# Kernel optimization log

Hardware: AMD Instinct MI355X
Metric: run time of the kernel (lower is better)

## Reference

```python
import jax, jax.numpy as jnp
import numpy as np

EPS = 1e-5
N, DEG, D, L = 50000, 16, 128, 2  # nodes, max_neighbor, embed_size, gnn_layer


def _log_map_zero(y):
    # Poincare ball log map at origin: atanh(||y||) * y / ||y||, with clamps
    n = jnp.linalg.norm(y, axis=-1, keepdims=True)
    nc = jnp.clip(n, EPS, 1.0 - EPS)
    return y * (jnp.arctanh(nc) / nc)


def _exp_map_zero(v):
    # Poincare ball exp map at origin: tanh(||v||) * v / ||v||
    n = jnp.linalg.norm(v, axis=-1, keepdims=True)
    nc = jnp.maximum(n, EPS)
    return v * (jnp.tanh(nc) / nc)


def setup_inputs() -> dict:
    key = jax.random.key(0)
    k1, k2, k3, k4, k5 = jax.random.split(key, 5)
    node_repr = jax.random.normal(k1, (N, D), jnp.float32) * 0.1
    adj = jax.random.randint(k2, (N, DEG), 0, N)
    weight = jax.random.normal(k3, (N, DEG), jnp.float32)
    mask = jnp.ones((N, 1), jnp.float32)
    # per-relation, per-layer message weights (2 relations: pos / neg edges)
    scale = 1.0 / np.sqrt(D)
    W_pos = jax.random.normal(k4, (L, D, D), jnp.float32) * scale
    W_neg = jax.random.normal(k5, (L, D, D), jnp.float32) * scale
    return {"node_repr": node_repr, "adj": adj, "weight": weight,
            "mask": mask, "W_pos": W_pos, "W_neg": W_neg}


def reference(node_repr, adj, weight, mask, W_pos, W_neg):
    # split_graph_by_negative_edge
    pos_m = (weight > 0).astype(weight.dtype)
    neg_m = (weight < 0).astype(weight.dtype)
    adjs = (adj * pos_m.astype(adj.dtype), adj * neg_m.astype(adj.dtype))
    ws = (weight * pos_m, (-weight) * neg_m)
    Ws = (W_pos, W_neg)

    x = node_repr
    for step in range(L):
        x = (_log_map_zero(x) if step > 0 else x) * mask
        combined = jnp.zeros_like(x)
        for a, w, W in zip(adjs, ws, Ws):
            msg = (x @ W[step]) * mask                    # [N, D]
            nb = msg[a.reshape(-1)].reshape(N, DEG, D)    # neighbor gather
            combined = combined + jnp.sum(w[..., None] * nb, axis=1)
        combined = combined * mask                        # dropout identity (eval)
        x = _exp_map_zero(combined) * mask
        x = jax.nn.relu(x) * mask                         # poincare activation
    return x
```

## Files before the change

### kernel.cpp

```cpp
#include <hip/hip_runtime.h>
#include <math.h>

#define DD 128
#define DEG 16
#define TM 16
#define LDST 136
#define EPSV 1e-5f

typedef _Float16 half4_t __attribute__((ext_vector_type(4)));
typedef _Float16 half8_t __attribute__((ext_vector_type(8)));
typedef float    f32x4   __attribute__((ext_vector_type(4)));

__global__ void prep(const float* __restrict__ x, const float* __restrict__ mask,
                     _Float16* __restrict__ x16, int n4, int xb,
                     const float* __restrict__ Wp, const float* __restrict__ Wn,
                     _Float16* __restrict__ WT)
{
    if ((int)blockIdx.x < xb) {
        int i = blockIdx.x * blockDim.x + threadIdx.x;
        if (i >= n4) return;
        float m = mask[i >> 5];
        float m2 = m * m;
        float4 v = ((const float4*)x)[i];
        half4_t h;
        h[0] = (_Float16)(v.x * m2); h[1] = (_Float16)(v.y * m2);
        h[2] = (_Float16)(v.z * m2); h[3] = (_Float16)(v.w * m2);
        ((half4_t*)x16)[i] = h;
    } else {
        int bid   = blockIdx.x - xb;
        int mat   = bid >> 3;
        int chunk = bid & 7;
        int l = mat >> 1, rel = mat & 1;
        const float* __restrict__ src = (rel ? Wn : Wp) + (size_t)l * DD * DD;
        _Float16* __restrict__ dst = WT + (size_t)mat * DD * DD;
        for (int o = chunk * 2048 + threadIdx.x; o < chunk * 2048 + 2048; o += 256) {
            int nn = o >> 7, kk = o & 127;
            dst[o] = (_Float16)src[kk * DD + nn];
        }
    }
}

__global__ __launch_bounds__(256, 4) void fused_layer(
    const _Float16* __restrict__ src16,
    const int*   __restrict__ adj, const float* __restrict__ wgt,
    const float* __restrict__ mask,
    const _Float16* __restrict__ WTp, const _Float16* __restrict__ WTn,
    float* __restrict__ dst_f32, _Float16* __restrict__ dst_f16,
    int n, int apply_logmap)
{
    __shared__ __align__(16) _Float16 aggP[TM][LDST];
    __shared__ __align__(16) _Float16 aggN[TM][LDST];
    __shared__ float partA[4][TM];
    __shared__ float partB[4][TM];

    const int row0 = blockIdx.x * TM;
    const int tid  = threadIdx.x;
    const int qw   = tid >> 4;
    const int l16  = tid & 15;

    float aP[8] = {0.f,0.f,0.f,0.f,0.f,0.f,0.f,0.f};
    float aN[8] = {0.f,0.f,0.f,0.f,0.f,0.f,0.f,0.f};
    const int node = row0 + qw;
    if (node < n) {
        const int*   __restrict__ arow = adj + (size_t)node * DEG;
        const float* __restrict__ wrow = wgt + (size_t)node * DEG;
        int   idxs[16];
        float ws[16];
        #pragma unroll
        for (int b = 0; b < 4; ++b) {
            int4   ia = ((const int4*)arow)[b];
            float4 wa = ((const float4*)wrow)[b];
            idxs[b*4+0] = ia.x; idxs[b*4+1] = ia.y; idxs[b*4+2] = ia.z; idxs[b*4+3] = ia.w;
            ws[b*4+0] = wa.x; ws[b*4+1] = wa.y; ws[b*4+2] = wa.z; ws[b*4+3] = wa.w;
        }
        half8_t v[16];
        #pragma unroll
        for (int j = 0; j < 16; ++j)
            v[j] = *(const half8_t*)(src16 + (size_t)idxs[j] * DD + l16 * 8);
        #pragma unroll
        for (int j = 0; j < 16; ++j) {
            float wp = fmaxf(ws[j], 0.f);
            float wn = fmaxf(-ws[j], 0.f);
            #pragma unroll
            for (int c = 0; c < 8; ++c) {
                float f = (float)v[j][c];
                aP[c] += wp * f;
                aN[c] += wn * f;
            }
        }
    }
    half8_t hP, hN;
    #pragma unroll
    for (int c = 0; c < 8; ++c) { hP[c] = (_Float16)aP[c]; hN[c] = (_Float16)aN[c]; }
    *(half8_t*)&aggP[qw][l16 * 8] = hP;
    *(half8_t*)&aggN[qw][l16 * 8] = hN;
    __syncthreads();

    const int wv2  = tid >> 6;
    const int l64  = tid & 63;
    const int l15  = l64 & 15;
    const int quad = l64 >> 4;

    half8_t aPf[4], aNf[4];
    #pragma unroll
    for (int kb = 0; kb < 4; ++kb) {
        aPf[kb] = *(const half8_t*)&aggP[l15][kb * 32 + quad * 8];
        aNf[kb] = *(const half8_t*)&aggN[l15][kb * 32 + quad * 8];
    }

    f32x4 acc[2];
    acc[0] = (f32x4){0.f, 0.f, 0.f, 0.f};
    acc[1] = (f32x4){0.f, 0.f, 0.f, 0.f};
    #pragma unroll
    for (int t = 0; t < 2; ++t) {
        const int nb = wv2 * 2 + t;
        const _Float16* bp = WTp + (size_t)(nb * 16 + l15) * DD + quad * 8;
        const _Float16* bn = WTn + (size_t)(nb * 16 + l15) * DD + quad * 8;
        #pragma unroll
        for (int kb = 0; kb < 4; ++kb) {
            acc[t] = __builtin_amdgcn_mfma_f32_16x16x32_f16(
                aPf[kb], *(const half8_t*)(bp + kb * 32), acc[t], 0, 0, 0);
            acc[t] = __builtin_amdgcn_mfma_f32_16x16x32_f16(
                aNf[kb], *(const half8_t*)(bn + kb * 32), acc[t], 0, 0, 0);
        }
    }

    float cv0[4], cv1[4], mr[4];
    #pragma unroll
    for (int r = 0; r < 4; ++r) {
        const int rl  = quad * 4 + r;
        const int row = row0 + rl;
        float m = (row < n) ? mask[row] : 0.f;
        mr[r] = m;
        float c0 = acc[0][r] * m, c1 = acc[1][r] * m;
        cv0[r] = c0; cv1[r] = c1;
        float p = c0 * c0 + c1 * c1;
        p += __shfl_xor(p, 1); p += __shfl_xor(p, 2);
        p += __shfl_xor(p, 4); p += __shfl_xor(p, 8);
        if (l15 == 0) partA[wv2][rl] = p;
    }
    __syncthreads();

    float x0[4], x1[4];
    #pragma unroll
    for (int r = 0; r < 4; ++r) {
        const int rl = quad * 4 + r;
        float c2 = partA[0][rl] + partA[1][rl] + partA[2][rl] + partA[3][rl];
        float nc = fmaxf(sqrtf(c2), EPSV);
        float sc = tanhf(nc) / nc;
        float m  = mr[r];
        float t0 = fmaxf(cv0[r] * sc * m, 0.f) * m;
        float t1 = fmaxf(cv1[r] * sc * m, 0.f) * m;
        x0[r] = t0; x1[r] = t1;
        if (apply_logmap) {
            float p = t0 * t0 + t1 * t1;
            p += __shfl_xor(p, 1); p += __shfl_xor(p, 2);
            p += __shfl_xor(p, 4); p += __shfl_xor(p, 8);
            if (l15 == 0) partB[wv2][rl] = p;
        }
    }

    if (apply_logmap) {
        __syncthreads();
        #pragma unroll
        for (int r = 0; r < 4; ++r) {
            const int rl  = quad * 4 + r;
            const int row = row0 + rl;
            if (row >= n) continue;
            float s2  = partB[0][rl] + partB[1][rl] + partB[2][rl] + partB[3][rl];
            float nc2 = fminf(fmaxf(sqrtf(s2), EPSV), 1.f - EPSV);
            float f = (atanhf(nc2) / nc2) * mr[r] * mr[r];
            _Float16* drow = dst_f16 + (size_t)row * DD + wv2 * 32 + l15;
            drow[0]  = (_Float16)(x0[r] * f);
            drow[16] = (_Float16)(x1[r] * f);
        }
    } else {
        #pragma unroll
        for (int r = 0; r < 4; ++r) {
            const int rl  = quad * 4 + r;
            const int row = row0 + rl;
            if (row >= n) continue;
            float* drow = dst_f32 + (size_t)row * DD + wv2 * 32 + l15;
            drow[0]  = x0[r];
            drow[16] = x1[r];
        }
    }
}

extern "C" void kernel_launch(void* const* d_in, const int* in_sizes, int n_in,
                              void* d_out, int out_size, void* d_ws, size_t ws_size,
                              hipStream_t stream)
{
    const float* node_repr = (const float*)d_in[0];
    const int*   adj       = (const int*)  d_in[1];
    const float* weight    = (const float*)d_in[2];
    const float* mask      = (const float*)d_in[3];
    const float* W_pos     = (const float*)d_in[4];
    const float* W_neg     = (const float*)d_in[5];

    const int n = in_sizes[0] / DD;

    _Float16* x16 = (_Float16*)d_ws;
    _Float16* y16 = x16 + (size_t)n * DD;
    _Float16* WT  = y16 + (size_t)n * DD;

    const int n4 = n * DD / 4;
    const int xb = (n4 + 255) / 256;
    prep<<<xb + 32, 256, 0, stream>>>(node_repr, mask, x16, n4, xb,
                                      W_pos, W_neg, WT);

    dim3 grid((n + TM - 1) / TM);
    fused_layer<<<grid, 256, 0, stream>>>(x16, adj, weight, mask,
                                          WT + 0 * DD * DD, WT + 1 * DD * DD,
                                          nullptr, y16, n, 1);
    fused_layer<<<grid, 256, 0, stream>>>(y16, adj, weight, mask,
                                          WT + 2 * DD * DD, WT + 3 * DD * DD,
                                          (float*)d_out, nullptr, n, 0);
}
```

Baseline: 188.1 us.

## Halve rows per block and spread each node's gather over 32 lanes

```diff
diff --git a/kernel.cpp b/kernel.cpp
--- a/kernel.cpp
+++ b/kernel.cpp
@@ -3,7 +3,8 @@
 
 #define DD 128
 #define DEG 16
-#define TM 16
+#define TMR 8
+#define TMP 16
 #define LDST 136
 #define EPSV 1e-5f
 
@@ -40,7 +41,7 @@
     }
 }
 
-__global__ __launch_bounds__(256, 4) void fused_layer(
+__global__ __launch_bounds__(256, 6) void fused_layer(
     const _Float16* __restrict__ src16,
     const int*   __restrict__ adj, const float* __restrict__ wgt,
     const float* __restrict__ mask,
@@ -48,52 +49,59 @@
     float* __restrict__ dst_f32, _Float16* __restrict__ dst_f16,
     int n, int apply_logmap)
 {
-    __shared__ __align__(16) _Float16 aggP[TM][LDST];
-    __shared__ __align__(16) _Float16 aggN[TM][LDST];
-    __shared__ float partA[4][TM];
-    __shared__ float partB[4][TM];
-
-    const int row0 = blockIdx.x * TM;
-    const int tid  = threadIdx.x;
-    const int qw   = tid >> 4;
-    const int l16  = tid & 15;
-
-    float aP[8] = {0.f,0.f,0.f,0.f,0.f,0.f,0.f,0.f};
-    float aN[8] = {0.f,0.f,0.f,0.f,0.f,0.f,0.f,0.f};
-    const int node = row0 + qw;
+    __shared__ __align__(16) _Float16 aggP[TMP][LDST];
+    __shared__ __align__(16) _Float16 aggN[TMP][LDST];
+    __shared__ float partA[4][TMP];
+    __shared__ float partB[4][TMP];
+
+    const int row0   = blockIdx.x * TMR;
+    const int tid    = threadIdx.x;
+    const int hw     = tid >> 5;
+    const int lane32 = tid & 31;
+
+    float aP[4] = {0.f, 0.f, 0.f, 0.f};
+    float aN[4] = {0.f, 0.f, 0.f, 0.f};
+    const int node = row0 + hw;
     if (node < n) {
         const int*   __restrict__ arow = adj + (size_t)node * DEG;
         const float* __restrict__ wrow = wgt + (size_t)node * DEG;
-        int   idxs[16];
-        float ws[16];
-        #pragma unroll
-        for (int b = 0; b < 4; ++b) {
-            int4   ia = ((const int4*)arow)[b];
-            float4 wa = ((const float4*)wrow)[b];
-            idxs[b*4+0] = ia.x; idxs[b*4+1] = ia.y; idxs[b*4+2] = ia.z; idxs[b*4+3] = ia.w;
-            ws[b*4+0] = wa.x; ws[b*4+1] = wa.y; ws[b*4+2] = wa.z; ws[b*4+3] = wa.w;
-        }
-        half8_t v[16];
+        int4   ia0 = ((const int4*)arow)[0];
+        int4   ia1 = ((const int4*)arow)[1];
+        int4   ia2 = ((const int4*)arow)[2];
+        int4   ia3 = ((const int4*)arow)[3];
+        float4 wa0 = ((const float4*)wrow)[0];
+        float4 wa1 = ((const float4*)wrow)[1];
+        float4 wa2 = ((const float4*)wrow)[2];
+        float4 wa3 = ((const float4*)wrow)[3];
+        const int idxs[16] = {ia0.x, ia0.y, ia0.z, ia0.w, ia1.x, ia1.y, ia1.z, ia1.w,
+                              ia2.x, ia2.y, ia2.z, ia2.w, ia3.x, ia3.y, ia3.z, ia3.w};
+        const float ws[16] = {wa0.x, wa0.y, wa0.z, wa0.w, wa1.x, wa1.y, wa1.z, wa1.w,
+                              wa2.x, wa2.y, wa2.z, wa2.w, wa3.x, wa3.y, wa3.z, wa3.w};
+        half4_t v[16];
         #pragma unroll
         for (int j = 0; j < 16; ++j)
-            v[j] = *(const half8_t*)(src16 + (size_t)idxs[j] * DD + l16 * 8);
+            v[j] = *(const half4_t*)(src16 + (size_t)idxs[j] * DD + lane32 * 4);
         #pragma unroll
         for (int j = 0; j < 16; ++j) {
             float wp = fmaxf(ws[j], 0.f);
             float wn = fmaxf(-ws[j], 0.f);
             #pragma unroll
-            for (int c = 0; c < 8; ++c) {
+            for (int c = 0; c < 4; ++c) {
                 float f = (float)v[j][c];
                 aP[c] += wp * f;
                 aN[c] += wn * f;
             }
         }
     }
-    half8_t hP, hN;
-    #pragma unroll
-    for (int c = 0; c < 8; ++c) { hP[c] = (_Float16)aP[c]; hN[c] = (_Float16)aN[c]; }
-    *(half8_t*)&aggP[qw][l16 * 8] = hP;
-    *(half8_t*)&aggN[qw][l16 * 8] = hN;
+    half4_t hP, hN, hz;
+    #pragma unroll
+    for (int c = 0; c < 4; ++c) {
+        hP[c] = (_Float16)aP[c]; hN[c] = (_Float16)aN[c]; hz[c] = (_Float16)0.f;
+    }
+    *(half4_t*)&aggP[hw][lane32 * 4] = hP;
+    *(half4_t*)&aggN[hw][lane32 * 4] = hN;
+    *(half4_t*)&aggP[TMR + hw][lane32 * 4] = hz;
+    *(half4_t*)&aggN[TMR + hw][lane32 * 4] = hz;
     __syncthreads();
 
     const int wv2  = tid >> 6;
@@ -130,7 +138,7 @@
     for (int r = 0; r < 4; ++r) {
         const int rl  = quad * 4 + r;
         const int row = row0 + rl;
-        float m = (row < n) ? mask[row] : 0.f;
+        float m = (rl < TMR && row < n) ? mask[row] : 0.f;
         mr[r] = m;
         float c0 = acc[0][r] * m, c1 = acc[1][r] * m;
         cv0[r] = c0; cv1[r] = c1;
@@ -166,7 +174,7 @@
         for (int r = 0; r < 4; ++r) {
             const int rl  = quad * 4 + r;
             const int row = row0 + rl;
-            if (row >= n) continue;
+            if (rl >= TMR || row >= n) continue;
             float s2  = partB[0][rl] + partB[1][rl] + partB[2][rl] + partB[3][rl];
             float nc2 = fminf(fmaxf(sqrtf(s2), EPSV), 1.f - EPSV);
             float f = (atanhf(nc2) / nc2) * mr[r] * mr[r];
@@ -179,7 +187,7 @@
         for (int r = 0; r < 4; ++r) {
             const int rl  = quad * 4 + r;
             const int row = row0 + rl;
-            if (row >= n) continue;
+            if (rl >= TMR || row >= n) continue;
             float* drow = dst_f32 + (size_t)row * DD + wv2 * 32 + l15;
             drow[0]  = x0[r];
             drow[16] = x1[r];
@@ -209,7 +217,7 @@
     prep<<<xb + 32, 256, 0, stream>>>(node_repr, mask, x16, n4, xb,
                                       W_pos, W_neg, WT);
 
-    dim3 grid((n + TM - 1) / TM);
+    dim3 grid((n + TMR - 1) / TMR);
     fused_layer<<<grid, 256, 0, stream>>>(x16, adj, weight, mask,
                                           WT + 0 * DD * DD, WT + 1 * DD * DD,
                                           nullptr, y16, n, 1);
```

After: 236.3 us. 1.26x slower.

## Split neighbor gather across waves by edge subsets with LDS partial-sum reduction

Applied to the files above, without the earlier changes.

```diff
diff --git a/kernel.cpp b/kernel.cpp
--- a/kernel.cpp
+++ b/kernel.cpp
@@ -48,64 +48,73 @@
     float* __restrict__ dst_f32, _Float16* __restrict__ dst_f16,
     int n, int apply_logmap)
 {
-    __shared__ __align__(16) _Float16 aggP[TM][LDST];
-    __shared__ __align__(16) _Float16 aggN[TM][LDST];
+    __shared__ __align__(16) _Float16 aggP[4][TM][LDST];
+    __shared__ __align__(16) _Float16 aggN[4][TM][LDST];
     __shared__ float partA[4][TM];
     __shared__ float partB[4][TM];
 
-    const int row0 = blockIdx.x * TM;
-    const int tid  = threadIdx.x;
-    const int qw   = tid >> 4;
-    const int l16  = tid & 15;
-
-    float aP[8] = {0.f,0.f,0.f,0.f,0.f,0.f,0.f,0.f};
-    float aN[8] = {0.f,0.f,0.f,0.f,0.f,0.f,0.f,0.f};
-    const int node = row0 + qw;
-    if (node < n) {
-        const int*   __restrict__ arow = adj + (size_t)node * DEG;
-        const float* __restrict__ wrow = wgt + (size_t)node * DEG;
-        int   idxs[16];
-        float ws[16];
-        #pragma unroll
-        for (int b = 0; b < 4; ++b) {
-            int4   ia = ((const int4*)arow)[b];
-            float4 wa = ((const float4*)wrow)[b];
-            idxs[b*4+0] = ia.x; idxs[b*4+1] = ia.y; idxs[b*4+2] = ia.z; idxs[b*4+3] = ia.w;
-            ws[b*4+0] = wa.x; ws[b*4+1] = wa.y; ws[b*4+2] = wa.z; ws[b*4+3] = wa.w;
-        }
-        half8_t v[16];
-        #pragma unroll
-        for (int j = 0; j < 16; ++j)
-            v[j] = *(const half8_t*)(src16 + (size_t)idxs[j] * DD + l16 * 8);
-        #pragma unroll
-        for (int j = 0; j < 16; ++j) {
-            float wp = fmaxf(ws[j], 0.f);
-            float wn = fmaxf(-ws[j], 0.f);
+    const int row0   = blockIdx.x * TM;
+    const int tid    = threadIdx.x;
+    const int wv     = tid >> 6;
+    const int l64    = tid & 63;
+    const int hw     = l64 >> 5;
+    const int lane32 = l64 & 31;
+
+    const int hrow0 = row0 + hw * 8;
+    const int mnode = hrow0 + (lane32 >> 2);
+    const int moff  = (mnode < n ? mnode : 0) * DEG + 4 * wv + (lane32 & 3);
+    int   mi = adj[moff];
+    float mw = wgt[moff];
+
+    half4_t v[32];
+    #pragma unroll
+    for (int i = 0; i < 8; ++i) {
+        #pragma unroll
+        for (int j = 0; j < 4; ++j) {
+            int idx = __shfl(mi, 4 * i + j, 32);
+            v[4 * i + j] = *(const half4_t*)(src16 + (size_t)idx * DD + lane32 * 4);
+        }
+    }
+    #pragma unroll
+    for (int i = 0; i < 8; ++i) {
+        float aP[4] = {0.f, 0.f, 0.f, 0.f};
+        float aN[4] = {0.f, 0.f, 0.f, 0.f};
+        #pragma unroll
+        for (int j = 0; j < 4; ++j) {
+            float w  = __shfl(mw, 4 * i + j, 32);
+            float wp = fmaxf(w, 0.f);
+            float wn = fmaxf(-w, 0.f);
             #pragma unroll
-            for (int c = 0; c < 8; ++c) {
-                float f = (float)v[j][c];
+            for (int c = 0; c < 4; ++c) {
+                float f = (float)v[4 * i + j][c];
                 aP[c] += wp * f;
                 aN[c] += wn * f;
             }
         }
-    }
-    half8_t hP, hN;
-    #pragma unroll
-    for (int c = 0; c < 8; ++c) { hP[c] = (_Float16)aP[c]; hN[c] = (_Float16)aN[c]; }
-    *(half8_t*)&aggP[qw][l16 * 8] = hP;
-    *(half8_t*)&aggN[qw][l16 * 8] = hN;
+        half4_t hP, hN;
+        #pragma unroll
+        for (int c = 0; c < 4; ++c) { hP[c] = (_Float16)aP[c]; hN[c] = (_Float16)aN[c]; }
+        const int r = hw * 8 + i;
+        *(half4_t*)&aggP[wv][r][lane32 * 4] = hP;
+        *(half4_t*)&aggN[wv][r][lane32 * 4] = hN;
+    }
     __syncthreads();
 
-    const int wv2  = tid >> 6;
-    const int l64  = tid & 63;
     const int l15  = l64 & 15;
     const int quad = l64 >> 4;
 
     half8_t aPf[4], aNf[4];
     #pragma unroll
     for (int kb = 0; kb < 4; ++kb) {
-        aPf[kb] = *(const half8_t*)&aggP[l15][kb * 32 + quad * 8];
-        aNf[kb] = *(const half8_t*)&aggN[l15][kb * 32 + quad * 8];
+        const int o = kb * 32 + quad * 8;
+        half8_t p = *(const half8_t*)&aggP[0][l15][o];
+        half8_t q = *(const half8_t*)&aggN[0][l15][o];
+        #pragma unroll
+        for (int w = 1; w < 4; ++w) {
+            p = p + *(const half8_t*)&aggP[w][l15][o];
+            q = q + *(const half8_t*)&aggN[w][l15][o];
+        }
+        aPf[kb] = p; aNf[kb] = q;
     }
 
     f32x4 acc[2];
@@ -113,7 +122,7 @@
     acc[1] = (f32x4){0.f, 0.f, 0.f, 0.f};
     #pragma unroll
     for (int t = 0; t < 2; ++t) {
-        const int nb = wv2 * 2 + t;
+        const int nb = wv * 2 + t;
         const _Float16* bp = WTp + (size_t)(nb * 16 + l15) * DD + quad * 8;
         const _Float16* bn = WTn + (size_t)(nb * 16 + l15) * DD + quad * 8;
         #pragma unroll
@@ -137,7 +146,7 @@
         float p = c0 * c0 + c1 * c1;
         p += __shfl_xor(p, 1); p += __shfl_xor(p, 2);
         p += __shfl_xor(p, 4); p += __shfl_xor(p, 8);
-        if (l15 == 0) partA[wv2][rl] = p;
+        if (l15 == 0) partA[wv][rl] = p;
     }
     __syncthreads();
 
@@ -156,7 +165,7 @@
             float p = t0 * t0 + t1 * t1;
             p += __shfl_xor(p, 1); p += __shfl_xor(p, 2);
             p += __shfl_xor(p, 4); p += __shfl_xor(p, 8);
-            if (l15 == 0) partB[wv2][rl] = p;
+            if (l15 == 0) partB[wv][rl] = p;
         }
     }
 
@@ -170,7 +179,7 @@
             float s2  = partB[0][rl] + partB[1][rl] + partB[2][rl] + partB[3][rl];
             float nc2 = fminf(fmaxf(sqrtf(s2), EPSV), 1.f - EPSV);
             float f = (atanhf(nc2) / nc2) * mr[r] * mr[r];
-            _Float16* drow = dst_f16 + (size_t)row * DD + wv2 * 32 + l15;
+            _Float16* drow = dst_f16 + (size_t)row * DD + wv * 32 + l15;
             drow[0]  = (_Float16)(x0[r] * f);
             drow[16] = (_Float16)(x1[r] * f);
         }
@@ -180,7 +189,7 @@
             const int rl  = quad * 4 + r;
             const int row = row0 + rl;
             if (row >= n) continue;
-            float* drow = dst_f32 + (size_t)row * DD + wv2 * 32 + l15;
+            float* drow = dst_f32 + (size_t)row * DD + wv * 32 + l15;
             drow[0]  = x0[r];
             drow[16] = x1[r];
         }
```

Measured after the change: 194.1 us. 1.03x slower.
